# Kernel tuning notes

Hardware: AMD Instinct MI355X
Metric: run time of the kernel (lower is better)

Reference implementation:

```python
import jax, jax.numpy as jnp
import numpy as np

B, L, S, V, I, H = 4096, 16, 512, 512, 512, 512  # batch, attn_length, attn_size, attn_vec_size, input_size, lstm hidden


def setup_inputs() -> dict:
    key = jax.random.key(0)
    ks = jax.random.split(key, 16)
    rn = lambda k, sh, sc=1.0: jax.random.normal(k, sh, dtype=jnp.float32) * sc
    return {
        "inputs": rn(ks[0], (B, I)),
        "cell_c": rn(ks[1], (B, H)),
        "cell_h": rn(ks[2], (B, H)),
        "attns": rn(ks[3], (B, S)),
        "attn_states": rn(ks[4], (B, L, S)),
        "W1": rn(ks[5], (I + S, I), 0.02),
        "b1": jnp.zeros((I,), jnp.float32),
        "Wx": rn(ks[6], (I, 4 * H), 0.02),
        "Wh": rn(ks[7], (H, 4 * H), 0.02),
        "b_lstm": jnp.zeros((4 * H,), jnp.float32),
        "W3": rn(ks[8], (2 * H, V), 0.02),
        "b3": jnp.zeros((V,), jnp.float32),
        "k": rn(ks[9], (1, 1, S, V), 0.02),
        "v": rn(ks[10], (1, 1, S, V), 0.02),
        "W2": rn(ks[11], (H + S, S), 0.02),
        "b2": jnp.zeros((S,), jnp.float32),
    }


def reference(inputs, cell_c, cell_h, attns, attn_states, W1, b1, Wx, Wh, b_lstm, W3, b3, k, v, W2, b2):
    # linear1: project [inputs; attns] -> cell input
    x = jnp.concatenate([inputs, attns], axis=1) @ W1 + b1  # [B, I]
    # LSTM cell step (gate order i, f, g, o)
    gates = x @ Wx + cell_h @ Wh + b_lstm  # [B, 4H]
    i, f, g, o = jnp.split(gates, 4, axis=1)
    c_new = jax.nn.sigmoid(f) * cell_c + jax.nn.sigmoid(i) * jnp.tanh(g)
    h_new = jax.nn.sigmoid(o) * jnp.tanh(c_new)
    # attention over attn_states with query = concat(new_state)
    query = jnp.concatenate([c_new, h_new], axis=1)  # [B, 2H]
    # 1x1 conv over [B, L, 1, S] with kernel [1,1,S,V] == matmul over S
    hf = jnp.einsum('bls,sv->blv', attn_states, k[0, 0])  # [B, L, V]
    y = query @ W3 + b3  # [B, V]
    t = jnp.tanh(hf + y[:, None, :])  # [B, L, V]
    # reduce_sum(v * t, [2,3]) with v [1,1,S,V] broadcast against t [B,L,1,V]
    # == einsum over V with v summed over its S axis (t independent of S axis)
    vsum = v[0, 0].sum(axis=0)  # [V]
    s = jnp.einsum('blv,v->bl', t, vsum)  # [B, L]
    a = jax.nn.softmax(s, axis=1)
    d = jnp.einsum('bl,bls->bs', a, attn_states)  # new_attns [B, S]
    # output projection on [cell_output; new_attns]
    output = jnp.concatenate([h_new, d], axis=1) @ W2 + b2  # [B, S]
    # shift attention window: drop oldest, append output
    new_attn_states = jnp.concatenate([attn_states[:, 1:, :], output[:, None, :]], axis=1)
    new_attn_states = new_attn_states.reshape(inputs.shape[0], L * S)
    return output, c_new, h_new, d, new_attn_states
```

## Files before the change

### kernel.cpp

```cpp
#include <hip/hip_runtime.h>
#include <hip/hip_bf16.h>
#include <math.h>

#define BB 4096
#define LL 16
#define SS 512
#define VV 512
#define II 512
#define HH 512

typedef __attribute__((ext_vector_type(4))) float f32x4;
typedef __attribute__((ext_vector_type(8))) short short8;

#define GLOBAL_AS __attribute__((address_space(1)))
#define LDS_AS __attribute__((address_space(3)))

__device__ __forceinline__ unsigned short f2bf(float f) {
    union { float f; unsigned u; } c; c.f = f;
    unsigned u = c.u + 0x7FFFu + ((c.u >> 16) & 1u);
    return (unsigned short)(u >> 16);
}
__device__ __forceinline__ float bf2f(unsigned short u) {
    union { unsigned u; float f; } c; c.u = ((unsigned)u) << 16;
    return c.f;
}
__device__ __forceinline__ float fast_tanh(float x) {
    return 1.f - 2.f / (__expf(2.f * x) + 1.f);
}

template<int MODE, int NF>
__global__ __launch_bounds__(256) void gemm_mfma(
    const ushort* __restrict__ A, const ushort* __restrict__ Bt,
    const float* __restrict__ bias, void* __restrict__ C, float* __restrict__ C2,
    int ldc, int M, int N, int K) {
    constexpr int BN = NF * 32;
    __shared__ ushort Als[128 * 64];
    __shared__ ushort Bls[BN * 64];
    const int tid  = threadIdx.x;
    const int lane = tid & 63;
    const int w    = tid >> 6;
    const int wm   = w >> 1, wn = w & 1;
    const int brow = blockIdx.y * 128;
    const int bcol = blockIdx.x * BN;
    f32x4 acc[4][NF] = {};
    const int nkt = K >> 6;
    for (int kt = 0; kt < nkt; ++kt) {
        __syncthreads();
        #pragma unroll
        for (int i = 0; i < 4; ++i) {
            int c0 = i * 256 + w * 64;
            int c  = c0 + lane;
            int row = c >> 3, sl = c & 7;
            const ushort* gp = A + (size_t)(brow + row) * K + kt * 64 + ((sl ^ (row & 7)) * 8);
            __builtin_amdgcn_global_load_lds((const GLOBAL_AS void*)gp,
                                             (LDS_AS void*)(Als + c0 * 8), 16, 0, 0);
        }
        #pragma unroll
        for (int i = 0; i < NF; ++i) {
            int c0 = i * 256 + w * 64;
            int c  = c0 + lane;
            int row = c >> 3, sl = c & 7;
            const ushort* gp = Bt + (size_t)(bcol + row) * K + kt * 64 + ((sl ^ (row & 7)) * 8);
            __builtin_amdgcn_global_load_lds((const GLOBAL_AS void*)gp,
                                             (LDS_AS void*)(Bls + c0 * 8), 16, 0, 0);
        }
        __syncthreads();
        const char* AlsB = (const char*)Als;
        const char* BlsB = (const char*)Bls;
        #pragma unroll
        for (int kh = 0; kh < 2; ++kh) {
            int ks = kh * 4 + (lane >> 4);
            short8 a[4], b[NF];
            #pragma unroll
            for (int m = 0; m < 4; ++m) {
                int row = wm * 64 + m * 16 + (lane & 15);
                a[m] = *(const short8*)(AlsB + (row * 8 + (ks ^ (row & 7))) * 16);
            }
            #pragma unroll
            for (int n = 0; n < NF; ++n) {
                int row = wn * (NF * 16) + n * 16 + (lane & 15);
                b[n] = *(const short8*)(BlsB + (row * 8 + (ks ^ (row & 7))) * 16);
            }
            #pragma unroll
            for (int m = 0; m < 4; ++m)
                #pragma unroll
                for (int n = 0; n < NF; ++n)
                    acc[m][n] = __builtin_amdgcn_mfma_f32_16x16x32_bf16(a[m], b[n], acc[m][n], 0, 0, 0);
        }
    }
    #pragma unroll
    for (int m = 0; m < 4; ++m)
        #pragma unroll
        for (int n = 0; n < NF; ++n)
            #pragma unroll
            for (int r = 0; r < 4; ++r) {
                int gm = brow + wm * 64 + m * 16 + (lane >> 4) * 4 + r;
                int gc = bcol + wn * (NF * 16) + n * 16 + (lane & 15);
                float v = acc[m][n][r] + bias[gc];
                if (MODE == 1) ((ushort*)C)[(size_t)gm * ldc + gc] = f2bf(v);
                else           ((float*)C)[(size_t)gm * ldc + gc] = v;
                if (MODE == 2) C2[((size_t)gm * 16 + 15) * 512 + gc] = v;
            }
}

__global__ __launch_bounds__(512) void gemm_score(
    const float* __restrict__ ASf, const ushort* __restrict__ Bt,
    const float* __restrict__ Y, const float* __restrict__ vsum,
    float* __restrict__ spart) {
    __shared__ ushort Als[128 * 64];
    __shared__ ushort Bls[256 * 64];
    __shared__ float sred[4][128];
    const int tid  = threadIdx.x;
    const int lane = tid & 63;
    const int w    = tid >> 6;
    const int wm   = w >> 2, wn = w & 3;
    const int l15  = lane & 15, l4 = lane >> 4;
    const int brow = blockIdx.y * 128;
    const int bcol = blockIdx.x * 256;
    f32x4 acc[4][4] = {};
    for (int kt = 0; kt < 8; ++kt) {
        __syncthreads();
        #pragma unroll
        for (int i = 0; i < 2; ++i) {
            int chunk = i * 512 + tid;
            int row = chunk >> 3, slot = chunk & 7;
            int gslot = slot ^ (row & 7);
            const float* gp = ASf + (size_t)(brow + row) * 512 + kt * 64 + gslot * 8;
            float4 f0 = *(const float4*)gp;
            float4 f1 = *(const float4*)(gp + 4);
            short8 pk;
            pk[0] = (short)f2bf(f0.x); pk[1] = (short)f2bf(f0.y);
            pk[2] = (short)f2bf(f0.z); pk[3] = (short)f2bf(f0.w);
            pk[4] = (short)f2bf(f1.x); pk[5] = (short)f2bf(f1.y);
            pk[6] = (short)f2bf(f1.z); pk[7] = (short)f2bf(f1.w);
            *(short8*)((char*)Als + chunk * 16) = pk;
        }
        #pragma unroll
        for (int i = 0; i < 4; ++i) {
            int c0 = i * 512 + w * 64;
            int c  = c0 + lane;
            int row = c >> 3, sl = c & 7;
            const ushort* gp = Bt + (size_t)(bcol + row) * 512 + kt * 64 + ((sl ^ (row & 7)) * 8);
            __builtin_amdgcn_global_load_lds((const GLOBAL_AS void*)gp,
                                             (LDS_AS void*)(Bls + c0 * 8), 16, 0, 0);
        }
        __syncthreads();
        const char* AlsB = (const char*)Als;
        const char* BlsB = (const char*)Bls;
        #pragma unroll
        for (int kh = 0; kh < 2; ++kh) {
            int ks = kh * 4 + l4;
            short8 a[4], b[4];
            #pragma unroll
            for (int m = 0; m < 4; ++m) {
                int row = wm * 64 + m * 16 + l15;
                a[m] = *(const short8*)(AlsB + (row * 8 + (ks ^ (row & 7))) * 16);
            }
            #pragma unroll
            for (int n = 0; n < 4; ++n) {
                int rowb = wn * 64 + n * 16 + l15;
                b[n] = *(const short8*)(BlsB + (rowb * 8 + (ks ^ (rowb & 7))) * 16);
            }
            #pragma unroll
            for (int m = 0; m < 4; ++m)
                #pragma unroll
                for (int n = 0; n < 4; ++n)
                    acc[m][n] = __builtin_amdgcn_mfma_f32_16x16x32_bf16(a[m], b[n], acc[m][n], 0, 0, 0);
        }
    }
    float part[4][4] = {};
    #pragma unroll
    for (int m = 0; m < 4; ++m) {
        int yb = (brow >> 4) + wm * 4 + m;
        #pragma unroll
        for (int n = 0; n < 4; ++n) {
            int gc = bcol + wn * 64 + n * 16 + l15;
            float yv = Y[(size_t)yb * 512 + gc];
            float vs = vsum[gc];
            #pragma unroll
            for (int r = 0; r < 4; ++r)
                part[m][r] += fast_tanh(acc[m][n][r] + yv) * vs;
        }
    }
    #pragma unroll
    for (int m = 0; m < 4; ++m)
        #pragma unroll
        for (int r = 0; r < 4; ++r) {
            float v = part[m][r];
            v += __shfl_xor(v, 1); v += __shfl_xor(v, 2);
            v += __shfl_xor(v, 4); v += __shfl_xor(v, 8);
            if (l15 == 0)
                sred[wn][wm * 64 + m * 16 + l4 * 4 + r] = v;
        }
    __syncthreads();
    if (tid < 128)
        spart[(size_t)blockIdx.x * (BB * LL) + brow + tid] =
            sred[0][tid] + sred[1][tid] + sred[2][tid] + sred[3][tid];
}

__global__ __launch_bounds__(128) void softmax_d3(
    const float* __restrict__ spart, const float* __restrict__ ASf,
    float* __restrict__ o_ns, float* __restrict__ o_d, ushort* __restrict__ A7) {
    const int b = blockIdx.x, tid = threadIdx.x;
    __shared__ float s_l[LL];
    if (tid < LL)
        s_l[tid] = spart[(size_t)b * LL + tid] + spart[(size_t)BB * LL + b * LL + tid];
    __syncthreads();
    float mx = -1e30f;
    #pragma unroll
    for (int l = 0; l < LL; ++l) mx = fmaxf(mx, s_l[l]);
    float wgt[LL]; float sum = 0.f;
    #pragma unroll
    for (int l = 0; l < LL; ++l) { wgt[l] = __expf(s_l[l] - mx); sum += wgt[l]; }
    const float inv = 1.f / sum;
    const int c = tid * 4;
    float d0 = 0.f, d1 = 0.f, d2 = 0.f, d3 = 0.f;
    #pragma unroll
    for (int l = 0; l < LL; ++l) {
        float4 v = *(const float4*)(ASf + ((size_t)b * LL + l) * 512 + c);
        if (l >= 1)
            *(float4*)(o_ns + ((size_t)b * LL + l - 1) * 512 + c) = v;
        d0 += wgt[l] * v.x; d1 += wgt[l] * v.y;
        d2 += wgt[l] * v.z; d3 += wgt[l] * v.w;
    }
    d0 *= inv; d1 *= inv; d2 *= inv; d3 *= inv;
    float4 dv; dv.x = d0; dv.y = d1; dv.z = d2; dv.w = d3;
    *(float4*)(o_d + (size_t)b * 512 + c) = dv;
    ushort4 uv; uv.x = f2bf(d0); uv.y = f2bf(d1); uv.z = f2bf(d2); uv.w = f2bf(d3);
    *(ushort4*)(A7 + (size_t)b * 1024 + 512 + c) = uv;
}

struct TrJob { const float* srcA; const float* srcB; int K0; ushort* dst; int N; int K; };
struct TrJobs { TrJob j[5]; };

__global__ void tr_cvt_all(TrJobs jobs) {
    TrJob jb = jobs.j[blockIdx.z];
    int bn = blockIdx.x, bk = blockIdx.y;
    if (bn * 32 >= jb.N || bk * 32 >= jb.K) return;
    __shared__ float tile[32][33];
    int tx = threadIdx.x, ty = threadIdx.y;
    #pragma unroll
    for (int j = 0; j < 4; ++j) {
        int k = bk * 32 + ty + j * 8;
        const float* s = (k < jb.K0) ? (jb.srcA + (size_t)k * jb.N)
                                     : (jb.srcB + (size_t)(k - jb.K0) * jb.N);
        tile[ty + j * 8][tx] = s[bn * 32 + tx];
    }
    __syncthreads();
    #pragma unroll
    for (int j = 0; j < 4; ++j) {
        int n = bn * 32 + ty + j * 8;
        jb.dst[(size_t)n * jb.K + bk * 32 + tx] = f2bf(tile[tx][ty + j * 8]);
    }
}

struct CvJobs { const float* src[3]; ushort* dst[3]; };
__global__ void cvt_all(CvJobs jobs) {
    const float* src = jobs.src[blockIdx.y];
    ushort* dst = jobs.dst[blockIdx.y];
    int idx = blockIdx.x * 256 + threadIdx.x;
    int i4 = idx & 127, row = idx >> 7;
    float4 v = *(const float4*)(src + (size_t)row * 512 + i4 * 4);
    ushort4 o; o.x = f2bf(v.x); o.y = f2bf(v.y); o.z = f2bf(v.z); o.w = f2bf(v.w);
    *(ushort4*)(dst + (size_t)row * 1024 + i4 * 4) = o;
}

__global__ void lstm_ew(const float4* __restrict__ g4, const float4* __restrict__ cc4,
                        float4* __restrict__ c4, float4* __restrict__ h4,
                        ushort* __restrict__ A4, ushort* __restrict__ A7) {
    int idx = blockIdx.x * 256 + threadIdx.x;
    int b = idx >> 7, q = idx & 127;
    const float4* g = g4 + (size_t)b * 512;
    float4 gi = g[q], gf = g[q + 128], gg = g[q + 256], go = g[q + 384];
    float4 cc = cc4[idx];
    float4 c, h;
    #pragma unroll
    for (int j = 0; j < 4; ++j) {
        float fi = ((const float*)&gi)[j], ff = ((const float*)&gf)[j];
        float fg = ((const float*)&gg)[j], fo = ((const float*)&go)[j];
        float si = 1.f / (1.f + __expf(-fi));
        float sf = 1.f / (1.f + __expf(-ff));
        float so = 1.f / (1.f + __expf(-fo));
        float cv = sf * ((const float*)&cc)[j] + si * tanhf(fg);
        ((float*)&c)[j] = cv;
        ((float*)&h)[j] = so * tanhf(cv);
    }
    c4[idx] = c; h4[idx] = h;
    ushort4 uc, uh;
    uc.x = f2bf(c.x); uc.y = f2bf(c.y); uc.z = f2bf(c.z); uc.w = f2bf(c.w);
    uh.x = f2bf(h.x); uh.y = f2bf(h.y); uh.z = f2bf(h.z); uh.w = f2bf(h.w);
    *(ushort4*)(A4 + (size_t)b * 1024 + q * 4) = uc;
    *(ushort4*)(A4 + (size_t)b * 1024 + 512 + q * 4) = uh;
    *(ushort4*)(A7 + (size_t)b * 1024 + q * 4) = uh;
}

__global__ void vsum_k(const float* __restrict__ Vm, float* __restrict__ out) {
    __shared__ float red[8][32];
    int tc = threadIdx.x & 31, ts = threadIdx.x >> 5;
    int v = blockIdx.x * 32 + tc;
    float acc = 0.f;
    for (int s = ts; s < SS; s += 8) acc += Vm[(size_t)s * VV + v];
    red[ts][tc] = acc;
    __syncthreads();
    if (ts == 0) {
        float t = 0.f;
        #pragma unroll
        for (int j = 0; j < 8; ++j) t += red[j][tc];
        out[v] = t;
    }
}

extern "C" void kernel_launch(void* const* d_in, const int* in_sizes, int n_in,
                              void* d_out, int out_size, void* d_ws, size_t ws_size,
                              hipStream_t stream) {
    const float* inputs      = (const float*)d_in[0];
    const float* cell_c      = (const float*)d_in[1];
    const float* cell_h      = (const float*)d_in[2];
    const float* attns       = (const float*)d_in[3];
    const float* attn_states = (const float*)d_in[4];
    const float* W1          = (const float*)d_in[5];
    const float* b1          = (const float*)d_in[6];
    const float* Wx          = (const float*)d_in[7];
    const float* Wh          = (const float*)d_in[8];
    const float* b_lstm      = (const float*)d_in[9];
    const float* W3          = (const float*)d_in[10];
    const float* b3          = (const float*)d_in[11];
    const float* kmat        = (const float*)d_in[12];
    const float* vmat        = (const float*)d_in[13];
    const float* W2          = (const float*)d_in[14];
    const float* b2          = (const float*)d_in[15];

    float* o_out = (float*)d_out;
    float* o_c   = o_out + (size_t)BB * HH;
    float* o_h   = o_c   + (size_t)BB * HH;
    float* o_d   = o_h   + (size_t)BB * HH;
    float* o_ns  = o_d   + (size_t)BB * SS;

    float* ws_gates = (float*)d_ws;
    float* ws_y     = ws_gates + (size_t)BB * 4 * HH;
    float* ws_vsum  = ws_y + (size_t)BB * VV;
    float* ws_spart = ws_vsum + VV;
    ushort* A1    = (ushort*)(ws_spart + (size_t)2 * BB * LL);
    ushort* A2    = A1 + (size_t)BB * 1024;
    ushort* A4    = A2 + (size_t)BB * 1024;
    ushort* A7    = A4 + (size_t)BB * 1024;
    ushort* W1t   = A7 + (size_t)BB * 1024;
    ushort* WxWht = W1t + (size_t)512 * 1024;
    ushort* W3t   = WxWht + (size_t)2048 * 1024;
    ushort* W2t   = W3t + (size_t)512 * 1024;
    ushort* kTt   = W2t + (size_t)512 * 1024;

    TrJobs tj;
    tj.j[0] = {W1, W1, 1024, W1t, 512, 1024};
    tj.j[1] = {Wx, Wh, 512, WxWht, 2048, 1024};
    tj.j[2] = {W3, W3, 1024, W3t, 512, 1024};
    tj.j[3] = {W2, W2, 1024, W2t, 512, 1024};
    tj.j[4] = {kmat, kmat, 512, kTt, 512, 512};
    tr_cvt_all<<<dim3(64, 32, 5), dim3(32, 8), 0, stream>>>(tj);
    CvJobs cj;
    cj.src[0] = inputs; cj.dst[0] = A1;
    cj.src[1] = attns;  cj.dst[1] = A1 + 512;
    cj.src[2] = cell_h; cj.dst[2] = A2 + 512;
    cvt_all<<<dim3(BB * 128 / 256, 3), 256, 0, stream>>>(cj);
    vsum_k<<<16, 256, 0, stream>>>(vmat, ws_vsum);

    gemm_mfma<1, 1><<<dim3(512 / 32, BB / 128), 256, 0, stream>>>(
        A1, W1t, b1, A2, nullptr, 1024, BB, 512, 1024);
    gemm_mfma<0, 4><<<dim3(2048 / 128, BB / 128), 256, 0, stream>>>(
        A2, WxWht, b_lstm, ws_gates, nullptr, 2048, BB, 2048, 1024);
    lstm_ew<<<BB * 128 / 256, 256, 0, stream>>>(
        (const float4*)ws_gates, (const float4*)cell_c,
        (float4*)o_c, (float4*)o_h, A4, A7);
    gemm_mfma<0, 1><<<dim3(512 / 32, BB / 128), 256, 0, stream>>>(
        A4, W3t, b3, ws_y, nullptr, 512, BB, 512, 1024);
    gemm_score<<<dim3(2, 512), 512, 0, stream>>>(
        attn_states, kTt, ws_y, ws_vsum, ws_spart);
    softmax_d3<<<BB, 128, 0, stream>>>(
        ws_spart, attn_states, o_ns, o_d, A7);
    gemm_mfma<2, 1><<<dim3(512 / 32, BB / 128), 256, 0, stream>>>(
        A7, W2t, b2, o_out, o_ns, 512, BB, 512, 1024);
}
```

Before: 247.8 us.

## Fuse attention score GEMM with softmax and context reduction per 4-batch tile

```diff
diff --git a/kernel.cpp b/kernel.cpp
--- a/kernel.cpp
+++ b/kernel.cpp
@@ -103,26 +103,25 @@
             }
 }
 
-__global__ __launch_bounds__(512) void gemm_score(
+__global__ __launch_bounds__(512, 4) void score_all(
     const float* __restrict__ ASf, const ushort* __restrict__ Bt,
     const float* __restrict__ Y, const float* __restrict__ vsum,
-    float* __restrict__ spart) {
-    __shared__ ushort Als[128 * 64];
-    __shared__ ushort Bls[256 * 64];
-    __shared__ float sred[4][128];
+    float* __restrict__ o_ns, float* __restrict__ o_d, ushort* __restrict__ A7) {
+    __shared__ ushort Als[64 * 64];
+    __shared__ ushort Bls[512 * 64];
+    __shared__ float sred[8][64];
+    __shared__ float s_lds[64];
     const int tid  = threadIdx.x;
     const int lane = tid & 63;
     const int w    = tid >> 6;
-    const int wm   = w >> 2, wn = w & 3;
     const int l15  = lane & 15, l4 = lane >> 4;
-    const int brow = blockIdx.y * 128;
-    const int bcol = blockIdx.x * 256;
+    const int brow = blockIdx.x * 64;
+    const int bg0  = brow >> 4;
     f32x4 acc[4][4] = {};
     for (int kt = 0; kt < 8; ++kt) {
         __syncthreads();
-        #pragma unroll
-        for (int i = 0; i < 2; ++i) {
-            int chunk = i * 512 + tid;
+        {
+            int chunk = tid;
             int row = chunk >> 3, slot = chunk & 7;
             int gslot = slot ^ (row & 7);
             const float* gp = ASf + (size_t)(brow + row) * 512 + kt * 64 + gslot * 8;
@@ -136,11 +135,11 @@
             *(short8*)((char*)Als + chunk * 16) = pk;
         }
         #pragma unroll
-        for (int i = 0; i < 4; ++i) {
+        for (int i = 0; i < 8; ++i) {
             int c0 = i * 512 + w * 64;
             int c  = c0 + lane;
             int row = c >> 3, sl = c & 7;
-            const ushort* gp = Bt + (size_t)(bcol + row) * 512 + kt * 64 + ((sl ^ (row & 7)) * 8);
+            const ushort* gp = Bt + (size_t)row * 512 + kt * 64 + ((sl ^ (row & 7)) * 8);
             __builtin_amdgcn_global_load_lds((const GLOBAL_AS void*)gp,
                                              (LDS_AS void*)(Bls + c0 * 8), 16, 0, 0);
         }
@@ -153,12 +152,12 @@
             short8 a[4], b[4];
             #pragma unroll
             for (int m = 0; m < 4; ++m) {
-                int row = wm * 64 + m * 16 + l15;
+                int row = m * 16 + l15;
                 a[m] = *(const short8*)(AlsB + (row * 8 + (ks ^ (row & 7))) * 16);
             }
             #pragma unroll
             for (int n = 0; n < 4; ++n) {
-                int rowb = wn * 64 + n * 16 + l15;
+                int rowb = w * 64 + n * 16 + l15;
                 b[n] = *(const short8*)(BlsB + (rowb * 8 + (ks ^ (rowb & 7))) * 16);
             }
             #pragma unroll
@@ -171,10 +170,10 @@
     float part[4][4] = {};
     #pragma unroll
     for (int m = 0; m < 4; ++m) {
-        int yb = (brow >> 4) + wm * 4 + m;
+        int yb = bg0 + m;
         #pragma unroll
         for (int n = 0; n < 4; ++n) {
-            int gc = bcol + wn * 64 + n * 16 + l15;
+            int gc = w * 64 + n * 16 + l15;
             float yv = Y[(size_t)yb * 512 + gc];
             float vs = vsum[gc];
             #pragma unroll
@@ -189,45 +188,43 @@
             float v = part[m][r];
             v += __shfl_xor(v, 1); v += __shfl_xor(v, 2);
             v += __shfl_xor(v, 4); v += __shfl_xor(v, 8);
-            if (l15 == 0)
-                sred[wn][wm * 64 + m * 16 + l4 * 4 + r] = v;
+            if (l15 == 0) sred[w][m * 16 + l4 * 4 + r] = v;
         }
     __syncthreads();
-    if (tid < 128)
-        spart[(size_t)blockIdx.x * (BB * LL) + brow + tid] =
-            sred[0][tid] + sred[1][tid] + sred[2][tid] + sred[3][tid];
-}
-
-__global__ __launch_bounds__(128) void softmax_d3(
-    const float* __restrict__ spart, const float* __restrict__ ASf,
-    float* __restrict__ o_ns, float* __restrict__ o_d, ushort* __restrict__ A7) {
-    const int b = blockIdx.x, tid = threadIdx.x;
-    __shared__ float s_l[LL];
-    if (tid < LL)
-        s_l[tid] = spart[(size_t)b * LL + tid] + spart[(size_t)BB * LL + b * LL + tid];
+    if (tid < 64) {
+        float v = 0.f;
+        #pragma unroll
+        for (int q = 0; q < 8; ++q) v += sred[q][tid];
+        s_lds[tid] = v;
+    }
     __syncthreads();
-    float mx = -1e30f;
-    #pragma unroll
-    for (int l = 0; l < LL; ++l) mx = fmaxf(mx, s_l[l]);
-    float wgt[LL]; float sum = 0.f;
-    #pragma unroll
-    for (int l = 0; l < LL; ++l) { wgt[l] = __expf(s_l[l] - mx); sum += wgt[l]; }
-    const float inv = 1.f / sum;
-    const int c = tid * 4;
-    float d0 = 0.f, d1 = 0.f, d2 = 0.f, d3 = 0.f;
-    #pragma unroll
-    for (int l = 0; l < LL; ++l) {
-        float4 v = *(const float4*)(ASf + ((size_t)b * LL + l) * 512 + c);
-        if (l >= 1)
-            *(float4*)(o_ns + ((size_t)b * LL + l - 1) * 512 + c) = v;
-        d0 += wgt[l] * v.x; d1 += wgt[l] * v.y;
-        d2 += wgt[l] * v.z; d3 += wgt[l] * v.w;
-    }
-    d0 *= inv; d1 *= inv; d2 *= inv; d3 *= inv;
-    float4 dv; dv.x = d0; dv.y = d1; dv.z = d2; dv.w = d3;
-    *(float4*)(o_d + (size_t)b * 512 + c) = dv;
-    ushort4 uv; uv.x = f2bf(d0); uv.y = f2bf(d1); uv.z = f2bf(d2); uv.w = f2bf(d3);
-    *(ushort4*)(A7 + (size_t)b * 1024 + 512 + c) = uv;
+
+    {
+        const int bat = w >> 1;
+        const int bg  = bg0 + bat;
+        const int c   = (w & 1) * 256 + lane * 4;
+        float mx = -1e30f;
+        #pragma unroll
+        for (int l = 0; l < LL; ++l) mx = fmaxf(mx, s_lds[bat * 16 + l]);
+        float wgt[LL]; float sum = 0.f;
+        #pragma unroll
+        for (int l = 0; l < LL; ++l) { wgt[l] = __expf(s_lds[bat * 16 + l] - mx); sum += wgt[l]; }
+        const float inv = 1.f / sum;
+        float d0 = 0.f, d1 = 0.f, d2 = 0.f, d3 = 0.f;
+        #pragma unroll
+        for (int l = 0; l < LL; ++l) {
+            float4 v = *(const float4*)(ASf + ((size_t)bg * 16 + l) * 512 + c);
+            if (l >= 1)
+                *(float4*)(o_ns + ((size_t)bg * 16 + l - 1) * 512 + c) = v;
+            d0 += wgt[l] * v.x; d1 += wgt[l] * v.y;
+            d2 += wgt[l] * v.z; d3 += wgt[l] * v.w;
+        }
+        d0 *= inv; d1 *= inv; d2 *= inv; d3 *= inv;
+        float4 dv; dv.x = d0; dv.y = d1; dv.z = d2; dv.w = d3;
+        *(float4*)(o_d + (size_t)bg * 512 + c) = dv;
+        ushort4 uv; uv.x = f2bf(d0); uv.y = f2bf(d1); uv.z = f2bf(d2); uv.w = f2bf(d3);
+        *(ushort4*)(A7 + (size_t)bg * 1024 + 512 + c) = uv;
+    }
 }
 
 struct TrJob { const float* srcA; const float* srcB; int K0; ushort* dst; int N; int K; };
@@ -339,8 +336,7 @@
     float* ws_gates = (float*)d_ws;
     float* ws_y     = ws_gates + (size_t)BB * 4 * HH;
     float* ws_vsum  = ws_y + (size_t)BB * VV;
-    float* ws_spart = ws_vsum + VV;
-    ushort* A1    = (ushort*)(ws_spart + (size_t)2 * BB * LL);
+    ushort* A1    = (ushort*)(ws_vsum + VV);
     ushort* A2    = A1 + (size_t)BB * 1024;
     ushort* A4    = A2 + (size_t)BB * 1024;
     ushort* A7    = A4 + (size_t)BB * 1024;
@@ -373,10 +369,8 @@
         (float4*)o_c, (float4*)o_h, A4, A7);
     gemm_mfma<0, 1><<<dim3(512 / 32, BB / 128), 256, 0, stream>>>(
         A4, W3t, b3, ws_y, nullptr, 512, BB, 512, 1024);
-    gemm_score<<<dim3(2, 512), 512, 0, stream>>>(
-        attn_states, kTt, ws_y, ws_vsum, ws_spart);
-    softmax_d3<<<BB, 128, 0, stream>>>(
-        ws_spart, attn_states, o_ns, o_d, A7);
+    score_all<<<BB * LL / 64, 512, 0, stream>>>(
+        attn_states, kTt, ws_y, ws_vsum, o_ns, o_d, A7);
     gemm_mfma<2, 1><<<dim3(512 / 32, BB / 128), 256, 0, stream>>>(
         A7, W2t, b2, o_out, o_ns, 512, BB, 512, 1024);
 }
```

Measured after the change: 235.4 us. 1.05x faster.
